# Kernel optimization log

Measured on AMD Instinct MI355X. Metric: run time of the kernel, lower is better.

The kernel has to match this reference:

```python
import jax, jax.numpy as jnp
import numpy as np

NUM_HEADS = 8

def setup_inputs() -> dict:
    key = jax.random.key(0)
    ks = jax.random.split(key, 12)
    T, B, C, D = 2048, 4, 512, 512
    s = 1.0 / np.sqrt(C)
    return {
        "key_in": jax.random.normal(ks[0], (T, B, C), jnp.float32),
        "value_in": jax.random.normal(ks[1], (T, B, C), jnp.float32),
        "query_in": jax.random.normal(ks[2], (T, B, C), jnp.float32),
        "Wk": jax.random.normal(ks[3], (C, D), jnp.float32) * s,
        "bk": jax.random.normal(ks[4], (D,), jnp.float32) * 0.01,
        "Wv": jax.random.normal(ks[5], (C, D), jnp.float32) * s,
        "bv": jax.random.normal(ks[6], (D,), jnp.float32) * 0.01,
        "Wq": jax.random.normal(ks[7], (C, D), jnp.float32) * s,
        "bq": jax.random.normal(ks[8], (D,), jnp.float32) * 0.01,
        "Wo": jax.random.normal(ks[9], (D, D), jnp.float32) * (1.0 / np.sqrt(D)),
        "bo": jax.random.normal(ks[10], (D,), jnp.float32) * 0.01,
    }

def reference(key_in, value_in, query_in, Wk, bk, Wv, bv, Wq, bq, Wo, bo):
    T, B, C = query_in.shape
    D = Wq.shape[1]
    H = NUM_HEADS
    hd = D // H
    scale = 1.0 / np.sqrt(hd).astype(np.float32)
    # Linear projections on (T, B, C) -> (T, B, D), then the original's
    # row-major view(B, -1, H, hd) followed by transpose(1, 2) -> (B, H, T, hd)
    def proj(x, W, b):
        y = x @ W + b                      # (T, B, D)
        return y.reshape(B, -1, H, hd).transpose(0, 2, 1, 3)  # (B, H, T, hd)
    q = proj(query_in, Wq, bq)
    k = proj(key_in, Wk, bk)
    v = proj(value_in, Wv, bv)
    scores = jnp.einsum("bhqd,bhkd->bhqk", q, k) * scale  # (B, H, T, T)
    attn = jax.nn.softmax(scores, axis=-1)
    x = jnp.einsum("bhqk,bhkd->bhqd", attn, v)            # (B, H, T, hd)
    x = x.transpose(0, 2, 1, 3).reshape(T, B, D)          # matches .view(T, B, d_model)
    return x @ Wo + bo
```

## Files before the change

### kernel.cpp

```cpp
#include <hip/hip_runtime.h>
#include <math.h>

#define MROWS 8192
#define DM    512
#define SEQL  2048
#define HDIM  64

typedef __attribute__((ext_vector_type(4))) float floatx4;
typedef _Float16 half2v __attribute__((ext_vector_type(2)));
typedef _Float16 half4v __attribute__((ext_vector_type(4)));
typedef _Float16 half8v __attribute__((ext_vector_type(8)));

#define CEXP 0.18033688011f

__device__ __forceinline__ void gll16(const void* g, void* l) {
    __builtin_amdgcn_global_load_lds(
        (const __attribute__((address_space(1))) unsigned int*)g,
        (__attribute__((address_space(3))) unsigned int*)l, 16, 0, 0);
}

__device__ __forceinline__ half4v pack4(float a, float b, float c, float d) {
    half2v lo = __builtin_bit_cast(half2v, __builtin_amdgcn_cvt_pkrtz(a, b));
    half2v hi = __builtin_bit_cast(half2v, __builtin_amdgcn_cvt_pkrtz(c, d));
    half4v r;
    r[0] = lo[0]; r[1] = lo[1]; r[2] = hi[0]; r[3] = hi[1];
    return r;
}

__global__ __launch_bounds__(256) void transw(const float* __restrict__ w0,
                                              const float* __restrict__ w1,
                                              const float* __restrict__ w2,
                                              const float* __restrict__ w3,
                                              _Float16* __restrict__ t0,
                                              _Float16* __restrict__ t1,
                                              _Float16* __restrict__ t2,
                                              _Float16* __restrict__ t3) {
    __shared__ float tile[32][33];
    const float* W = blockIdx.z == 0 ? w0 : (blockIdx.z == 1 ? w1 : (blockIdx.z == 2 ? w2 : w3));
    _Float16* T = blockIdx.z == 0 ? t0 : (blockIdx.z == 1 ? t1 : (blockIdx.z == 2 ? t2 : t3));
    const float sc = (blockIdx.z == 0) ? CEXP : 1.0f;
    const int tx = threadIdx.x & 31, ty = threadIdx.x >> 5;
    const int x = blockIdx.x * 32 + tx;
    const int y0 = blockIdx.y * 32;
#pragma unroll
    for (int i = 0; i < 4; ++i)
        tile[ty + i * 8][tx] = W[(size_t)(y0 + ty + i * 8) * DM + x];
    __syncthreads();
    const int xo = y0 + tx;
#pragma unroll
    for (int i = 0; i < 4; ++i)
        T[(size_t)(blockIdx.x * 32 + ty + i * 8) * DM + xo] = (_Float16)(tile[tx][ty + i * 8] * sc);
}

__global__ __launch_bounds__(256, 3) void proj_gemm(
        const float* __restrict__ q32, const float* __restrict__ k32, const float* __restrict__ v32,
        const _Float16* __restrict__ Wq, const _Float16* __restrict__ Wk, const _Float16* __restrict__ Wv,
        const float* __restrict__ bq, const float* __restrict__ bk, const float* __restrict__ bv,
        _Float16* __restrict__ Qo, _Float16* __restrict__ Ko, _Float16* __restrict__ Vto) {
    __shared__ _Float16 As[128 * 64];
    __shared__ _Float16 Bs[128 * 64];
    const int z = blockIdx.z;
    const float* A32    = z == 0 ? q32 : (z == 1 ? k32 : v32);
    const _Float16* Bt  = z == 0 ? Wq : (z == 1 ? Wk : Wv);
    const float* bias   = z == 0 ? bq : (z == 1 ? bk : bv);
    const float bscale  = z == 0 ? CEXP : 1.0f;

    const int tid = threadIdx.x;
    const int w = tid >> 6, wr = w >> 1, wc = w & 1;
    const int l15 = tid & 15, quad = (tid & 63) >> 4;
    const int m0 = blockIdx.x * 128, n0 = blockIdx.y * 128;

    const int arow = tid >> 1, ah = tid & 1;
    const float* Asrc = &A32[(size_t)(m0 + arow) * DM + ah * 32];
    _Float16* Adst = &As[arow * 64];
    const int asw = arow & 7;

    floatx4 acc[4][4];
#pragma unroll
    for (int i = 0; i < 4; ++i)
#pragma unroll
        for (int j = 0; j < 4; ++j) acc[i][j] = (floatx4){0.f, 0.f, 0.f, 0.f};

    for (int kt = 0; kt < DM / 64; ++kt) {
        __syncthreads();
        floatx4 f[8];
        {
            const float* s = Asrc + (size_t)kt * 64;
#pragma unroll
            for (int q = 0; q < 8; ++q) f[q] = *(const floatx4*)&s[q * 4];
        }
#pragma unroll
        for (int i = 0; i < 4; ++i) {
            const int c = i * 256 + tid;
            const int row = c >> 3, g = c & 7;
            const int kg = g ^ (row & 7);
            gll16(&Bt[(size_t)(n0 + row) * DM + kt * 64 + kg * 8], &Bs[c * 8]);
        }
#pragma unroll
        for (int t = 0; t < 4; ++t) {
            half8v o;
            o[0] = (_Float16)f[2 * t][0]; o[1] = (_Float16)f[2 * t][1];
            o[2] = (_Float16)f[2 * t][2]; o[3] = (_Float16)f[2 * t][3];
            o[4] = (_Float16)f[2 * t + 1][0]; o[5] = (_Float16)f[2 * t + 1][1];
            o[6] = (_Float16)f[2 * t + 1][2]; o[7] = (_Float16)f[2 * t + 1][3];
            const int g = ah * 4 + t;
            *(half8v*)&Adst[(g ^ asw) * 8] = o;
        }
        __syncthreads();
#pragma unroll
        for (int ks = 0; ks < 2; ++ks) {
            half8v af[4], bf[4];
#pragma unroll
            for (int i = 0; i < 4; ++i) {
                const int row = wr * 64 + i * 16 + l15;
                af[i] = *(const half8v*)&As[row * 64 + (((ks * 4 + quad)) ^ (row & 7)) * 8];
            }
#pragma unroll
            for (int j = 0; j < 4; ++j) {
                const int row = wc * 64 + j * 16 + l15;
                bf[j] = *(const half8v*)&Bs[row * 64 + (((ks * 4 + quad)) ^ (row & 7)) * 8];
            }
#pragma unroll
            for (int i = 0; i < 4; ++i)
#pragma unroll
                for (int j = 0; j < 4; ++j)
                    acc[i][j] = __builtin_amdgcn_mfma_f32_16x16x32_f16(af[i], bf[j], acc[i][j], 0, 0, 0);
        }
    }
#pragma unroll
    for (int j = 0; j < 4; ++j) {
        const int col = n0 + wc * 64 + j * 16 + l15;
        const float bv4 = bias[col] * bscale;
#pragma unroll
        for (int i = 0; i < 4; ++i) {
            const int rb = m0 + wr * 64 + i * 16 + quad * 4;
            if (z == 2) {
                const int g = rb >> 11, seq = rb & 2047;
                half4v pv;
#pragma unroll
                for (int r = 0; r < 4; ++r) pv[r] = (_Float16)(acc[i][j][r] + bv4);
                *(half4v*)&Vto[((size_t)g * DM + col) * SEQL + seq] = pv;
            } else {
                _Float16* oh = z == 0 ? Qo : Ko;
#pragma unroll
                for (int r = 0; r < 4; ++r)
                    oh[(size_t)(rb + r) * DM + col] = (_Float16)(acc[i][j][r] + bv4);
            }
        }
    }
}

__global__ __launch_bounds__(256, 4) void out_gemm(
        const _Float16* __restrict__ O16,
        const _Float16* __restrict__ Wo, const float* __restrict__ bo,
        float* __restrict__ out) {
    __shared__ _Float16 Bs[256 * 64];
    __shared__ _Float16 As[32 * 64];
    const int tid = threadIdx.x;
    const int w = tid >> 6;
    const int l15 = tid & 15, quad = (tid & 63) >> 4;
    const int n0 = blockIdx.x * 256, m0 = blockIdx.y * 32;

    const int arow = tid >> 3, ag = tid & 7;
    const int akg = ag ^ (arow & 7);

    floatx4 acc[2][4];
#pragma unroll
    for (int i = 0; i < 2; ++i)
#pragma unroll
        for (int j = 0; j < 4; ++j) acc[i][j] = (floatx4){0.f, 0.f, 0.f, 0.f};

    for (int kt = 0; kt < DM / 64; ++kt) {
        __syncthreads();
#pragma unroll
        for (int i = 0; i < 8; ++i) {
            const int c = i * 256 + tid;
            const int row = c >> 3, g = c & 7;
            const int kg = g ^ (row & 7);
            gll16(&Wo[(size_t)(n0 + row) * DM + kt * 64 + kg * 8], &Bs[c * 8]);
        }
        gll16(&O16[(size_t)(m0 + arow) * DM + kt * 64 + akg * 8], &As[tid * 8]);
        __syncthreads();
#pragma unroll
        for (int ks = 0; ks < 2; ++ks) {
            half8v af[2], bfr[4];
#pragma unroll
            for (int i = 0; i < 2; ++i) {
                const int row = i * 16 + l15;
                af[i] = *(const half8v*)&As[row * 64 + ((ks * 4 + quad) ^ (row & 7)) * 8];
            }
#pragma unroll
            for (int j = 0; j < 4; ++j) {
                const int row = w * 64 + j * 16 + l15;
                bfr[j] = *(const half8v*)&Bs[row * 64 + ((ks * 4 + quad) ^ (row & 7)) * 8];
            }
#pragma unroll
            for (int i = 0; i < 2; ++i)
#pragma unroll
                for (int j = 0; j < 4; ++j)
                    acc[i][j] = __builtin_amdgcn_mfma_f32_16x16x32_f16(af[i], bfr[j], acc[i][j], 0, 0, 0);
        }
    }
#pragma unroll
    for (int j = 0; j < 4; ++j) {
        const int col = n0 + w * 64 + j * 16 + l15;
        const float bv4 = bo[col];
#pragma unroll
        for (int i = 0; i < 2; ++i) {
            const int rb = m0 + i * 16 + quad * 4;
#pragma unroll
            for (int r = 0; r < 4; ++r)
                out[(size_t)(rb + r) * DM + col] = acc[i][j][r] + bv4;
        }
    }
}

__global__ __launch_bounds__(256, 4) void attn_mfma(const _Float16* __restrict__ Q16,
                                                    const _Float16* __restrict__ K16,
                                                    const _Float16* __restrict__ Vt,
                                                    _Float16* __restrict__ O16) {
    __shared__ _Float16 Ks[2][64 * 64];
    __shared__ _Float16 Vs[2][64 * 64];

    const int tid  = threadIdx.x;
    const int lane = tid & 63;
    const int l15  = lane & 15;
    const int quad = lane >> 4;

    const int idl  = blockIdx.y * 16 + blockIdx.x;
    const int swz  = (idl & 7) * 64 + (idl >> 3);
    const int pair = swz >> 4;
    const int grp  = pair >> 3;
    const int h    = pair & 7;
    const int q0   = (swz & 15) * 128;
    const int rQ   = grp * SEQL + q0 + (tid >> 6) * 32;
    const int cb   = h * HDIM;
    const int NIT  = SEQL / 64;

    const _Float16* Kbase = K16 + (size_t)grp * SEQL * DM + cb;
    const _Float16* Vbase = Vt + (size_t)grp * DM * SEQL + (size_t)cb * SEQL;

    half8v qf[2][2];
#pragma unroll
    for (int qt = 0; qt < 2; ++qt)
#pragma unroll
        for (int ks = 0; ks < 2; ++ks)
            qf[qt][ks] = *(const half8v*)&Q16[(size_t)(rQ + qt * 16 + l15) * DM + cb + ks * 32 + quad * 8];

    floatx4 oacc[2][4], lacc[2];
#pragma unroll
    for (int qt = 0; qt < 2; ++qt) {
        lacc[qt] = (floatx4){0.f, 0.f, 0.f, 0.f};
#pragma unroll
        for (int dt = 0; dt < 4; ++dt) oacc[qt][dt] = (floatx4){0.f, 0.f, 0.f, 0.f};
    }
    half4v ones;
    ones[0] = (_Float16)1.f; ones[1] = (_Float16)1.f; ones[2] = (_Float16)1.f; ones[3] = (_Float16)1.f;

#define STAGE(KT, B)                                                            \
    {                                                                           \
        _Float16* ksb = &Ks[B][0];                                              \
        _Float16* vsb = &Vs[B][0];                                              \
        _Pragma("unroll")                                                       \
        for (int i_ = 0; i_ < 4; ++i_) {                                        \
            const int c_ = i_ * 256 + tid;                                      \
            if (c_ < 512) {                                                     \
                const int key_ = c_ >> 3, g_ = c_ & 7;                          \
                const int dg_ = g_ ^ (key_ & 7);                                \
                gll16(&Kbase[(size_t)((KT) * 64 + key_) * DM + dg_ * 8],        \
                      &ksb[c_ * 8]);                                            \
            } else {                                                            \
                const int cv_ = c_ - 512;                                       \
                const int d_ = cv_ >> 3, g_ = cv_ & 7;                          \
                const int kg_ = g_ ^ (d_ & 7);                                  \
                gll16(&Vbase[(size_t)d_ * SEQL + (KT) * 64 + kg_ * 8],          \
                      &vsb[cv_ * 8]);                                           \
            }                                                                   \
        }                                                                       \
    }

    STAGE(0, 0)

    for (int it = 0; it < NIT; ++it) {
        const int cur = it & 1;
        __syncthreads();
        if (it + 1 < NIT) STAGE(it + 1, cur ^ 1)

        const _Float16* ksb = &Ks[cur][0];
        const _Float16* vsb = &Vs[cur][0];

        floatx4 st[4][2];
#pragma unroll
        for (int ktile = 0; ktile < 4; ++ktile) {
            const int key = ktile * 16 + l15;
            const half8v kf0 = *(const half8v*)&ksb[key * 64 + ((0 + quad) ^ (key & 7)) * 8];
            const half8v kf1 = *(const half8v*)&ksb[key * 64 + ((4 + quad) ^ (key & 7)) * 8];
#pragma unroll
            for (int qt = 0; qt < 2; ++qt) {
                floatx4 z = {0.f, 0.f, 0.f, 0.f};
                z = __builtin_amdgcn_mfma_f32_16x16x32_f16(kf0, qf[qt][0], z, 0, 0, 0);
                st[ktile][qt] = __builtin_amdgcn_mfma_f32_16x16x32_f16(kf1, qf[qt][1], z, 0, 0, 0);
            }
        }

        half4v pa[4][2];
#pragma unroll
        for (int ktile = 0; ktile < 4; ++ktile)
#pragma unroll
            for (int qt = 0; qt < 2; ++qt)
                pa[ktile][qt] = pack4(__builtin_amdgcn_exp2f(st[ktile][qt][0]),
                                      __builtin_amdgcn_exp2f(st[ktile][qt][1]),
                                      __builtin_amdgcn_exp2f(st[ktile][qt][2]),
                                      __builtin_amdgcn_exp2f(st[ktile][qt][3]));

#pragma unroll
        for (int qt = 0; qt < 2; ++qt)
#pragma unroll
            for (int ktile = 0; ktile < 4; ++ktile)
                lacc[qt] = __builtin_amdgcn_mfma_f32_16x16x16f16(pa[ktile][qt], ones, lacc[qt], 0, 0, 0);

#pragma unroll
        for (int dt = 0; dt < 4; ++dt) {
            const int d = dt * 16 + l15;
#pragma unroll
            for (int ktile = 0; ktile < 4; ++ktile) {
                const int G = ktile * 2 + (quad >> 1);
                const int slot = G ^ (d & 7);
                const half4v vf = *(const half4v*)&vsb[d * 64 + slot * 8 + (quad & 1) * 4];
#pragma unroll
                for (int qt = 0; qt < 2; ++qt)
                    oacc[qt][dt] = __builtin_amdgcn_mfma_f32_16x16x16f16(pa[ktile][qt], vf, oacc[qt][dt], 0, 0, 0);
            }
        }
    }

#pragma unroll
    for (int qt = 0; qt < 2; ++qt)
#pragma unroll
        for (int r = 0; r < 4; ++r) {
            const int qrow = rQ + qt * 16 + quad * 4 + r;
            const size_t rowoff = (size_t)qrow * DM + cb;
            const float inv = 1.0f / lacc[qt][r];
#pragma unroll
            for (int dt = 0; dt < 4; ++dt)
                O16[rowoff + dt * 16 + l15] = (_Float16)(oacc[qt][dt][r] * inv);
        }
}

extern "C" void kernel_launch(void* const* d_in, const int* in_sizes, int n_in,
                              void* d_out, int out_size, void* d_ws, size_t ws_size,
                              hipStream_t stream) {
    const float* key_in   = (const float*)d_in[0];
    const float* value_in = (const float*)d_in[1];
    const float* query_in = (const float*)d_in[2];
    const float* Wk = (const float*)d_in[3];
    const float* bk = (const float*)d_in[4];
    const float* Wv = (const float*)d_in[5];
    const float* bv = (const float*)d_in[6];
    const float* Wq = (const float*)d_in[7];
    const float* bq = (const float*)d_in[8];
    const float* Wo = (const float*)d_in[9];
    const float* bo = (const float*)d_in[10];
    float* out = (float*)d_out;

    const size_t MAT = (size_t)MROWS * DM;
    _Float16* Q16  = (_Float16*)d_ws;
    _Float16* K16  = Q16 + MAT;
    _Float16* Vtb  = K16 + MAT;
    _Float16* Wqt  = Vtb + MAT;
    _Float16* Wkt  = Wqt + DM * DM;
    _Float16* Wvt  = Wkt + DM * DM;
    _Float16* Wot  = Wvt + DM * DM;
    _Float16* O16  = Wot + DM * DM;

    const dim3 blk(256);

    transw<<<dim3(16, 16, 4), blk, 0, stream>>>(Wq, Wk, Wv, Wo, Wqt, Wkt, Wvt, Wot);

    proj_gemm<<<dim3(MROWS / 128, DM / 128, 3), blk, 0, stream>>>(
        query_in, key_in, value_in, Wqt, Wkt, Wvt, bq, bk, bv, Q16, K16, Vtb);

    attn_mfma<<<dim3(SEQL / 128, 32), blk, 0, stream>>>(Q16, K16, Vtb, O16);

    out_gemm<<<dim3(2, MROWS / 32), blk, 0, stream>>>(O16, Wot, bo, out);
}
```

Baseline: 198.7 us.

## Use 8 waves per attention block with 16 query rows per wave

New measurement: 201.2 us. About the same (+1.3%).

```diff
diff --git a/kernel.cpp b/kernel.cpp
--- a/kernel.cpp
+++ b/kernel.cpp
@@ -215,7 +215,7 @@
     }
 }
 
-__global__ __launch_bounds__(256, 4) void attn_mfma(const _Float16* __restrict__ Q16,
+__global__ __launch_bounds__(512, 4) void attn_mfma(const _Float16* __restrict__ Q16,
                                                     const _Float16* __restrict__ K16,
                                                     const _Float16* __restrict__ Vt,
                                                     _Float16* __restrict__ O16) {
@@ -224,6 +224,7 @@
 
     const int tid  = threadIdx.x;
     const int lane = tid & 63;
+    const int wid  = tid >> 6;
     const int l15  = lane & 15;
     const int quad = lane >> 4;
 
@@ -233,27 +234,22 @@
     const int grp  = pair >> 3;
     const int h    = pair & 7;
     const int q0   = (swz & 15) * 128;
-    const int rQ   = grp * SEQL + q0 + (tid >> 6) * 32;
+    const int rQ   = grp * SEQL + q0 + wid * 16;
     const int cb   = h * HDIM;
     const int NIT  = SEQL / 64;
 
     const _Float16* Kbase = K16 + (size_t)grp * SEQL * DM + cb;
     const _Float16* Vbase = Vt + (size_t)grp * DM * SEQL + (size_t)cb * SEQL;
 
-    half8v qf[2][2];
-#pragma unroll
-    for (int qt = 0; qt < 2; ++qt)
-#pragma unroll
-        for (int ks = 0; ks < 2; ++ks)
-            qf[qt][ks] = *(const half8v*)&Q16[(size_t)(rQ + qt * 16 + l15) * DM + cb + ks * 32 + quad * 8];
-
-    floatx4 oacc[2][4], lacc[2];
-#pragma unroll
-    for (int qt = 0; qt < 2; ++qt) {
-        lacc[qt] = (floatx4){0.f, 0.f, 0.f, 0.f};
-#pragma unroll
-        for (int dt = 0; dt < 4; ++dt) oacc[qt][dt] = (floatx4){0.f, 0.f, 0.f, 0.f};
-    }
+    half8v qf[2];
+#pragma unroll
+    for (int ks = 0; ks < 2; ++ks)
+        qf[ks] = *(const half8v*)&Q16[(size_t)(rQ + l15) * DM + cb + ks * 32 + quad * 8];
+
+    floatx4 oacc[4], lacc;
+    lacc = (floatx4){0.f, 0.f, 0.f, 0.f};
+#pragma unroll
+    for (int dt = 0; dt < 4; ++dt) oacc[dt] = (floatx4){0.f, 0.f, 0.f, 0.f};
     half4v ones;
     ones[0] = (_Float16)1.f; ones[1] = (_Float16)1.f; ones[2] = (_Float16)1.f; ones[3] = (_Float16)1.f;
 
@@ -262,8 +258,8 @@
         _Float16* ksb = &Ks[B][0];                                              \
         _Float16* vsb = &Vs[B][0];                                              \
         _Pragma("unroll")                                                       \
-        for (int i_ = 0; i_ < 4; ++i_) {                                        \
-            const int c_ = i_ * 256 + tid;                                      \
+        for (int i_ = 0; i_ < 2; ++i_) {                                        \
+            const int c_ = i_ * 512 + tid;                                      \
             if (c_ < 512) {                                                     \
                 const int key_ = c_ >> 3, g_ = c_ & 7;                          \
                 const int dg_ = g_ ^ (key_ & 7);                                \
@@ -289,35 +285,28 @@
         const _Float16* ksb = &Ks[cur][0];
         const _Float16* vsb = &Vs[cur][0];
 
-        floatx4 st[4][2];
+        floatx4 st[4];
 #pragma unroll
         for (int ktile = 0; ktile < 4; ++ktile) {
             const int key = ktile * 16 + l15;
             const half8v kf0 = *(const half8v*)&ksb[key * 64 + ((0 + quad) ^ (key & 7)) * 8];
             const half8v kf1 = *(const half8v*)&ksb[key * 64 + ((4 + quad) ^ (key & 7)) * 8];
-#pragma unroll
-            for (int qt = 0; qt < 2; ++qt) {
-                floatx4 z = {0.f, 0.f, 0.f, 0.f};
-                z = __builtin_amdgcn_mfma_f32_16x16x32_f16(kf0, qf[qt][0], z, 0, 0, 0);
-                st[ktile][qt] = __builtin_amdgcn_mfma_f32_16x16x32_f16(kf1, qf[qt][1], z, 0, 0, 0);
-            }
-        }
-
-        half4v pa[4][2];
+            floatx4 z = {0.f, 0.f, 0.f, 0.f};
+            z = __builtin_amdgcn_mfma_f32_16x16x32_f16(kf0, qf[0], z, 0, 0, 0);
+            st[ktile] = __builtin_amdgcn_mfma_f32_16x16x32_f16(kf1, qf[1], z, 0, 0, 0);
+        }
+
+        half4v pa[4];
 #pragma unroll
         for (int ktile = 0; ktile < 4; ++ktile)
-#pragma unroll
-            for (int qt = 0; qt < 2; ++qt)
-                pa[ktile][qt] = pack4(__builtin_amdgcn_exp2f(st[ktile][qt][0]),
-                                      __builtin_amdgcn_exp2f(st[ktile][qt][1]),
-                                      __builtin_amdgcn_exp2f(st[ktile][qt][2]),
-                                      __builtin_amdgcn_exp2f(st[ktile][qt][3]));
-
-#pragma unroll
-        for (int qt = 0; qt < 2; ++qt)
-#pragma unroll
-            for (int ktile = 0; ktile < 4; ++ktile)
-                lacc[qt] = __builtin_amdgcn_mfma_f32_16x16x16f16(pa[ktile][qt], ones, lacc[qt], 0, 0, 0);
+            pa[ktile] = pack4(__builtin_amdgcn_exp2f(st[ktile][0]),
+                              __builtin_amdgcn_exp2f(st[ktile][1]),
+                              __builtin_amdgcn_exp2f(st[ktile][2]),
+                              __builtin_amdgcn_exp2f(st[ktile][3]));
+
+#pragma unroll
+        for (int ktile = 0; ktile < 4; ++ktile)
+            lacc = __builtin_amdgcn_mfma_f32_16x16x16f16(pa[ktile], ones, lacc, 0, 0, 0);
 
 #pragma unroll
         for (int dt = 0; dt < 4; ++dt) {
@@ -327,24 +316,20 @@
                 const int G = ktile * 2 + (quad >> 1);
                 const int slot = G ^ (d & 7);
                 const half4v vf = *(const half4v*)&vsb[d * 64 + slot * 8 + (quad & 1) * 4];
-#pragma unroll
-                for (int qt = 0; qt < 2; ++qt)
-                    oacc[qt][dt] = __builtin_amdgcn_mfma_f32_16x16x16f16(pa[ktile][qt], vf, oacc[qt][dt], 0, 0, 0);
-            }
-        }
-    }
-
-#pragma unroll
-    for (int qt = 0; qt < 2; ++qt)
-#pragma unroll
-        for (int r = 0; r < 4; ++r) {
-            const int qrow = rQ + qt * 16 + quad * 4 + r;
-            const size_t rowoff = (size_t)qrow * DM + cb;
-            const float inv = 1.0f / lacc[qt][r];
-#pragma unroll
-            for (int dt = 0; dt < 4; ++dt)
-                O16[rowoff + dt * 16 + l15] = (_Float16)(oacc[qt][dt][r] * inv);
-        }
+                oacc[dt] = __builtin_amdgcn_mfma_f32_16x16x16f16(pa[ktile], vf, oacc[dt], 0, 0, 0);
+            }
+        }
+    }
+
+#pragma unroll
+    for (int r = 0; r < 4; ++r) {
+        const int qrow = rQ + quad * 4 + r;
+        const size_t rowoff = (size_t)qrow * DM + cb;
+        const float inv = 1.0f / lacc[r];
+#pragma unroll
+        for (int dt = 0; dt < 4; ++dt)
+            O16[rowoff + dt * 16 + l15] = (_Float16)(oacc[dt][r] * inv);
+    }
 }
 
 extern "C" void kernel_launch(void* const* d_in, const int* in_sizes, int n_in,
@@ -380,7 +365,7 @@
     proj_gemm<<<dim3(MROWS / 128, DM / 128, 3), blk, 0, stream>>>(
         query_in, key_in, value_in, Wqt, Wkt, Wvt, bq, bk, bv, Q16, K16, Vtb);
 
-    attn_mfma<<<dim3(SEQL / 128, 32), blk, 0, stream>>>(Q16, K16, Vtb, O16);
+    attn_mfma<<<dim3(SEQL / 128, 32), dim3(512), 0, stream>>>(Q16, K16, Vtb, O16);
 
     out_gemm<<<dim3(2, MROWS / 32), blk, 0, stream>>>(O16, Wot, bo, out);
 }
```

## Switch attention kernel to 32x32x16 MFMA tiles with lane-swap P repacking

Applied to the files above, without the earlier changes.

Result: no change. 201.0 us (+1.2%).

```diff
diff --git a/kernel.cpp b/kernel.cpp
--- a/kernel.cpp
+++ b/kernel.cpp
@@ -7,6 +7,7 @@
 #define HDIM  64
 
 typedef __attribute__((ext_vector_type(4))) float floatx4;
+typedef __attribute__((ext_vector_type(16))) float floatx16;
 typedef _Float16 half2v __attribute__((ext_vector_type(2)));
 typedef _Float16 half4v __attribute__((ext_vector_type(4)));
 typedef _Float16 half8v __attribute__((ext_vector_type(8)));
@@ -17,14 +18,6 @@
     __builtin_amdgcn_global_load_lds(
         (const __attribute__((address_space(1))) unsigned int*)g,
         (__attribute__((address_space(3))) unsigned int*)l, 16, 0, 0);
-}
-
-__device__ __forceinline__ half4v pack4(float a, float b, float c, float d) {
-    half2v lo = __builtin_bit_cast(half2v, __builtin_amdgcn_cvt_pkrtz(a, b));
-    half2v hi = __builtin_bit_cast(half2v, __builtin_amdgcn_cvt_pkrtz(c, d));
-    half4v r;
-    r[0] = lo[0]; r[1] = lo[1]; r[2] = hi[0]; r[3] = hi[1];
-    return r;
 }
 
 __global__ __launch_bounds__(256) void transw(const float* __restrict__ w0,
@@ -215,7 +208,7 @@
     }
 }
 
-__global__ __launch_bounds__(256, 4) void attn_mfma(const _Float16* __restrict__ Q16,
+__global__ __launch_bounds__(256, 2) void attn_mfma(const _Float16* __restrict__ Q16,
                                                     const _Float16* __restrict__ K16,
                                                     const _Float16* __restrict__ Vt,
                                                     _Float16* __restrict__ O16) {
@@ -224,8 +217,10 @@
 
     const int tid  = threadIdx.x;
     const int lane = tid & 63;
-    const int l15  = lane & 15;
-    const int quad = lane >> 4;
+    const int wid  = tid >> 6;
+    const int l31  = lane & 31;
+    const int hi   = lane >> 5;
+    const int swapaddr = ((lane ^ 32) << 2);
 
     const int idl  = blockIdx.y * 16 + blockIdx.x;
     const int swz  = (idl & 7) * 64 + (idl >> 3);
@@ -233,29 +228,24 @@
     const int grp  = pair >> 3;
     const int h    = pair & 7;
     const int q0   = (swz & 15) * 128;
-    const int rQ   = grp * SEQL + q0 + (tid >> 6) * 32;
+    const int rQb  = grp * SEQL + q0 + wid * 32;
     const int cb   = h * HDIM;
     const int NIT  = SEQL / 64;
 
     const _Float16* Kbase = K16 + (size_t)grp * SEQL * DM + cb;
     const _Float16* Vbase = Vt + (size_t)grp * DM * SEQL + (size_t)cb * SEQL;
 
-    half8v qf[2][2];
-#pragma unroll
-    for (int qt = 0; qt < 2; ++qt)
-#pragma unroll
-        for (int ks = 0; ks < 2; ++ks)
-            qf[qt][ks] = *(const half8v*)&Q16[(size_t)(rQ + qt * 16 + l15) * DM + cb + ks * 32 + quad * 8];
-
-    floatx4 oacc[2][4], lacc[2];
-#pragma unroll
-    for (int qt = 0; qt < 2; ++qt) {
-        lacc[qt] = (floatx4){0.f, 0.f, 0.f, 0.f};
-#pragma unroll
-        for (int dt = 0; dt < 4; ++dt) oacc[qt][dt] = (floatx4){0.f, 0.f, 0.f, 0.f};
-    }
-    half4v ones;
-    ones[0] = (_Float16)1.f; ones[1] = (_Float16)1.f; ones[2] = (_Float16)1.f; ones[3] = (_Float16)1.f;
+    half8v qf[4];
+#pragma unroll
+    for (int t = 0; t < 4; ++t)
+        qf[t] = *(const half8v*)&Q16[(size_t)(rQb + l31) * DM + cb + t * 16 + hi * 8];
+
+    floatx16 oacc[2], lacc;
+#pragma unroll
+    for (int r = 0; r < 16; ++r) { oacc[0][r] = 0.f; oacc[1][r] = 0.f; lacc[r] = 0.f; }
+    half8v ones8;
+#pragma unroll
+    for (int e = 0; e < 8; ++e) ones8[e] = (_Float16)1.f;
 
 #define STAGE(KT, B)                                                            \
     {                                                                           \
@@ -289,62 +279,65 @@
         const _Float16* ksb = &Ks[cur][0];
         const _Float16* vsb = &Vs[cur][0];
 
-        floatx4 st[4][2];
-#pragma unroll
-        for (int ktile = 0; ktile < 4; ++ktile) {
-            const int key = ktile * 16 + l15;
-            const half8v kf0 = *(const half8v*)&ksb[key * 64 + ((0 + quad) ^ (key & 7)) * 8];
-            const half8v kf1 = *(const half8v*)&ksb[key * 64 + ((4 + quad) ^ (key & 7)) * 8];
-#pragma unroll
-            for (int qt = 0; qt < 2; ++qt) {
-                floatx4 z = {0.f, 0.f, 0.f, 0.f};
-                z = __builtin_amdgcn_mfma_f32_16x16x32_f16(kf0, qf[qt][0], z, 0, 0, 0);
-                st[ktile][qt] = __builtin_amdgcn_mfma_f32_16x16x32_f16(kf1, qf[qt][1], z, 0, 0, 0);
-            }
-        }
-
-        half4v pa[4][2];
-#pragma unroll
-        for (int ktile = 0; ktile < 4; ++ktile)
-#pragma unroll
-            for (int qt = 0; qt < 2; ++qt)
-                pa[ktile][qt] = pack4(__builtin_amdgcn_exp2f(st[ktile][qt][0]),
-                                      __builtin_amdgcn_exp2f(st[ktile][qt][1]),
-                                      __builtin_amdgcn_exp2f(st[ktile][qt][2]),
-                                      __builtin_amdgcn_exp2f(st[ktile][qt][3]));
-
-#pragma unroll
-        for (int qt = 0; qt < 2; ++qt)
-#pragma unroll
-            for (int ktile = 0; ktile < 4; ++ktile)
-                lacc[qt] = __builtin_amdgcn_mfma_f32_16x16x16f16(pa[ktile][qt], ones, lacc[qt], 0, 0, 0);
-
-#pragma unroll
-        for (int dt = 0; dt < 4; ++dt) {
-            const int d = dt * 16 + l15;
-#pragma unroll
-            for (int ktile = 0; ktile < 4; ++ktile) {
-                const int G = ktile * 2 + (quad >> 1);
-                const int slot = G ^ (d & 7);
-                const half4v vf = *(const half4v*)&vsb[d * 64 + slot * 8 + (quad & 1) * 4];
-#pragma unroll
-                for (int qt = 0; qt < 2; ++qt)
-                    oacc[qt][dt] = __builtin_amdgcn_mfma_f32_16x16x16f16(pa[ktile][qt], vf, oacc[qt][dt], 0, 0, 0);
-            }
-        }
-    }
-
-#pragma unroll
-    for (int qt = 0; qt < 2; ++qt)
-#pragma unroll
-        for (int r = 0; r < 4; ++r) {
-            const int qrow = rQ + qt * 16 + quad * 4 + r;
-            const size_t rowoff = (size_t)qrow * DM + cb;
-            const float inv = 1.0f / lacc[qt][r];
-#pragma unroll
-            for (int dt = 0; dt < 4; ++dt)
-                O16[rowoff + dt * 16 + l15] = (_Float16)(oacc[qt][dt][r] * inv);
-        }
+        floatx16 st[2];
+#pragma unroll
+        for (int g = 0; g < 2; ++g) {
+            const int key = g * 32 + l31;
+            floatx16 z;
+#pragma unroll
+            for (int r = 0; r < 16; ++r) z[r] = 0.f;
+#pragma unroll
+            for (int t = 0; t < 4; ++t) {
+                const half8v kf = *(const half8v*)&ksb[key * 64 + ((t * 2 + hi) ^ (key & 7)) * 8];
+                z = __builtin_amdgcn_mfma_f32_32x32x16_f16(kf, qf[t], z, 0, 0, 0);
+            }
+            st[g] = z;
+        }
+
+#pragma unroll
+        for (int g = 0; g < 2; ++g) {
+            float e[16];
+#pragma unroll
+            for (int r = 0; r < 16; ++r) e[r] = __builtin_amdgcn_exp2f(st[g][r]);
+            unsigned c[8];
+#pragma unroll
+            for (int a = 0; a < 4; ++a) {
+                c[2 * a]     = __builtin_bit_cast(unsigned, __builtin_amdgcn_cvt_pkrtz(e[4 * a + 0], e[4 * a + 1]));
+                c[2 * a + 1] = __builtin_bit_cast(unsigned, __builtin_amdgcn_cvt_pkrtz(e[4 * a + 2], e[4 * a + 3]));
+            }
+            unsigned x[8];
+#pragma unroll
+            for (int i = 0; i < 8; ++i)
+                x[i] = (unsigned)__builtin_amdgcn_ds_bpermute(swapaddr, (int)c[i]);
+#pragma unroll
+            for (int kb = 0; kb < 2; ++kb) {
+                union { unsigned u[4]; half8v hv; } pu;
+                pu.u[0] = hi ? x[4 * kb + 2] : c[4 * kb + 0];
+                pu.u[1] = hi ? x[4 * kb + 3] : c[4 * kb + 1];
+                pu.u[2] = hi ? c[4 * kb + 2] : x[4 * kb + 0];
+                pu.u[3] = hi ? c[4 * kb + 3] : x[4 * kb + 1];
+                const half8v pa = pu.hv;
+                lacc = __builtin_amdgcn_mfma_f32_32x32x16_f16(pa, ones8, lacc, 0, 0, 0);
+                const int KB = g * 2 + kb;
+#pragma unroll
+                for (int dh = 0; dh < 2; ++dh) {
+                    const int d = dh * 32 + l31;
+                    const half8v vf = *(const half8v*)&vsb[d * 64 + ((KB * 2 + hi) ^ (d & 7)) * 8];
+                    oacc[dh] = __builtin_amdgcn_mfma_f32_32x32x16_f16(pa, vf, oacc[dh], 0, 0, 0);
+                }
+            }
+        }
+    }
+
+#pragma unroll
+    for (int r = 0; r < 16; ++r) {
+        const int qrow = rQb + (r & 3) + 8 * (r >> 2) + 4 * hi;
+        const float inv = 1.0f / lacc[r];
+        const size_t rowoff = (size_t)qrow * DM + cb;
+#pragma unroll
+        for (int dh = 0; dh < 2; ++dh)
+            O16[rowoff + dh * 32 + l31] = (_Float16)(oacc[dh][r] * inv);
+    }
 }
 
 extern "C" void kernel_launch(void* const* d_in, const int* in_sizes, int n_in,
```
